# Kernel tuning notes

Measured on AMD Instinct MI355X. Metric: run time of the kernel, lower is better.

The kernel has to match this reference:

```python
import jax, jax.numpy as jnp
import numpy as np

B, H, S, D = 2, 16, 2048, 64

def setup_inputs() -> dict:
    key = jax.random.key(0)
    kq, kk, kv, km = jax.random.split(key, 4)
    q = jax.random.normal(kq, (B, H, S, D), dtype=jnp.float32)
    k = jax.random.normal(kk, (B, H, S, D), dtype=jnp.float32)
    v = jax.random.normal(kv, (B, H, S, D), dtype=jnp.float32)
    mask = jax.random.randint(km, (1, 1, S, S), 0, 2, dtype=jnp.int32)
    return {"q": q, "k": k, "v": v, "mask": mask}

def reference(q, k, v, mask):
    d_k = q.shape[-1]
    # scores: [B,H,S,S] = q @ k^T / sqrt(d_k)
    scores = jnp.einsum('bhqd,bhkd->bhqk', q, k) / jnp.sqrt(jnp.float32(d_k))
    scores = jnp.where(mask == 0, -jnp.inf, scores)
    score = jax.nn.softmax(scores, axis=-1)
    output = jnp.einsum('bhqk,bhkd->bhqd', score, v)
    return (output, score)
```

## Files before the change

kernel.cpp:

```cpp
#include <hip/hip_runtime.h>
#include <hip/hip_bf16.h>


#define BH 32
#define SEQ 2048
#define DIM 64

typedef __attribute__((ext_vector_type(8))) short short8;
typedef __attribute__((ext_vector_type(4))) float floatx4;
typedef __attribute__((ext_vector_type(4))) unsigned int uintx4;

__device__ __forceinline__ short f2bf(float f) {
    unsigned u = __builtin_bit_cast(unsigned, f);
    unsigned r = u + 0x7fffu + ((u >> 16) & 1u);
    return (short)(r >> 16);
}

__device__ __forceinline__ unsigned pack2bf(float lo, float hi) {
    unsigned ul = __builtin_bit_cast(unsigned, lo);
    unsigned uh = __builtin_bit_cast(unsigned, hi);
    ul = ul + 0x7fffu + ((ul >> 16) & 1u);
    uh = uh + 0x7fffu + ((uh >> 16) & 1u);
    return (ul >> 16) | (uh & 0xffff0000u);
}

__device__ __forceinline__ short8 cvt_frag(float4 a, float4 b) {
    short8 r;
    r[0] = f2bf(a.x); r[1] = f2bf(a.y); r[2] = f2bf(a.z); r[3] = f2bf(a.w);
    r[4] = f2bf(b.x); r[5] = f2bf(b.y); r[6] = f2bf(b.z); r[7] = f2bf(b.w);
    return r;
}

__device__ __forceinline__ short8 load_frag_f32(const float* p) {
    float4 a = *reinterpret_cast<const float4*>(p);
    float4 b = *reinterpret_cast<const float4*>(p + 4);
    return cvt_frag(a, b);
}


__global__ void maskbits_kernel(const int* __restrict__ mask,
                                unsigned long long* __restrict__ bits) {
    int tid = blockIdx.x * blockDim.x + threadIdx.x;
    unsigned long long b = __ballot(mask[tid] != 0);
    if ((threadIdx.x & 63) == 0) bits[tid >> 6] = b;
}

__global__ void cvt_k_kernel(const float* __restrict__ k, short* __restrict__ kb) {
    size_t i = ((size_t)blockIdx.x * blockDim.x + threadIdx.x) * 8;
    float4 a = *reinterpret_cast<const float4*>(k + i);
    float4 b = *reinterpret_cast<const float4*>(k + i + 4);
    *reinterpret_cast<short8*>(kb + i) = cvt_frag(a, b);
}

__global__ __launch_bounds__(256) void cvt_vt_kernel(const float* __restrict__ v,
                                                     short* __restrict__ vt) {
    __shared__ float tile[64][65];
    const int bh = blockIdx.y;
    const int sblk = blockIdx.x;
    const int t = threadIdx.x;
    const float* vb = v + ((size_t)bh * SEQ + sblk * 64) * DIM;
#pragma unroll
    for (int it = 0; it < 4; ++it) {
        int row = it * 16 + (t >> 4);
        int c4 = (t & 15) * 4;
        float4 a = *reinterpret_cast<const float4*>(vb + row * DIM + c4);
        tile[row][c4] = a.x; tile[row][c4 + 1] = a.y;
        tile[row][c4 + 2] = a.z; tile[row][c4 + 3] = a.w;
    }
    __syncthreads();
    short* vo = vt + (size_t)bh * SEQ * DIM;
#pragma unroll
    for (int it = 0; it < 2; ++it) {
        int c = it * 256 + t;
        int d = c >> 3;
        int s8 = (c & 7) * 8;
        short8 r;
#pragma unroll
        for (int j = 0; j < 8; ++j) r[j] = f2bf(tile[s8 + j][d]);
        *reinterpret_cast<short8*>(vo + (size_t)d * SEQ + sblk * 64 + s8) = r;
    }
}


__global__ __launch_bounds__(256, 8) void attn_fast(
    const float* __restrict__ q, const short* __restrict__ kb,
    const short* __restrict__ vt, const unsigned int* __restrict__ maskbits,
    float* __restrict__ out, float* __restrict__ score)
{
    __shared__ float lpart[4][16];
    __shared__ float ocomb[2][4][4][64];

    const int bh   = blockIdx.y;
    const int qb   = blockIdx.x;
    const int wave = threadIdx.x >> 6;
    const int lane = threadIdx.x & 63;
    const int quad = lane >> 4;
    const int n    = lane & 15;
    const int half = wave & 1;
    const int q0   = qb * 32 + (wave >> 1) * 16;
    const int q4   = quad * 4;
    const int cp0  = half * (SEQ / 64);
    const int cp1  = cp0 + (SEQ / 64);

    const float* qbase = q  + (size_t)bh * SEQ * DIM;
    const short* kbb   = kb + (size_t)bh * SEQ * DIM;
    const short* vtb   = vt + (size_t)bh * SEQ * DIM;

    const short8 qf0 = load_frag_f32(qbase + (size_t)(q0 + n) * DIM + quad * 8);
    const short8 qf1 = load_frag_f32(qbase + (size_t)(q0 + n) * DIM + 32 + quad * 8);

    const short* kn  = kbb + (size_t)n * DIM + quad * 8;
    const short* vn0 = vtb + (size_t)n * SEQ + quad * 8;
    const unsigned int* mr = maskbits + (size_t)(q0 + n) * (SEQ / 32);
    float* sb = score + (size_t)bh * SEQ * SEQ + (size_t)(q0 + n) * SEQ + q4;

    float lsum = 0.f;
    for (int cp = cp0; cp < cp1; ++cp) {
        const int cbase = cp * 32;
        const short* k0 = kn + (size_t)cbase * DIM;
        short8 kf00 = *reinterpret_cast<const short8*>(k0);
        short8 kf01 = *reinterpret_cast<const short8*>(k0 + 32);
        short8 kf10 = *reinterpret_cast<const short8*>(k0 + 16 * DIM);
        short8 kf11 = *reinterpret_cast<const short8*>(k0 + 16 * DIM + 32);
        floatx4 a0 = {0.f, 0.f, 0.f, 0.f}, a1 = {0.f, 0.f, 0.f, 0.f};
        a0 = __builtin_amdgcn_mfma_f32_16x16x32_bf16(kf00, qf0, a0, 0, 0, 0);
        a0 = __builtin_amdgcn_mfma_f32_16x16x32_bf16(kf01, qf1, a0, 0, 0, 0);
        a1 = __builtin_amdgcn_mfma_f32_16x16x32_bf16(kf10, qf0, a1, 0, 0, 0);
        a1 = __builtin_amdgcn_mfma_f32_16x16x32_bf16(kf11, qf1, a1, 0, 0, 0);
        const unsigned w = mr[cp];
#pragma unroll
        for (int r = 0; r < 4; ++r) {
            float e0 = ((w >> (q4 + r)) & 1u)      ? __expf(a0[r] * 0.125f) : 0.f;
            float e1 = ((w >> (q4 + r + 16)) & 1u) ? __expf(a1[r] * 0.125f) : 0.f;
            lsum += e0 + e1;
        }
    }
    lsum += __shfl_xor(lsum, 16, 64);
    lsum += __shfl_xor(lsum, 32, 64);
    if (lane < 16) lpart[wave][lane] = lsum;
    __syncthreads();
    const float invl = 1.0f / (lsum + lpart[wave ^ 1][n]);

    floatx4 o[4];
#pragma unroll
    for (int t = 0; t < 4; ++t) o[t] = (floatx4){0.f, 0.f, 0.f, 0.f};

    for (int cp = cp0; cp < cp1; ++cp) {
        const int cbase = cp * 32;
        const short* k0 = kn + (size_t)cbase * DIM;
        short8 kf00 = *reinterpret_cast<const short8*>(k0);
        short8 kf01 = *reinterpret_cast<const short8*>(k0 + 32);
        short8 kf10 = *reinterpret_cast<const short8*>(k0 + 16 * DIM);
        short8 kf11 = *reinterpret_cast<const short8*>(k0 + 16 * DIM + 32);
        floatx4 a0 = {0.f, 0.f, 0.f, 0.f}, a1 = {0.f, 0.f, 0.f, 0.f};
        a0 = __builtin_amdgcn_mfma_f32_16x16x32_bf16(kf00, qf0, a0, 0, 0, 0);
        a0 = __builtin_amdgcn_mfma_f32_16x16x32_bf16(kf01, qf1, a0, 0, 0, 0);
        a1 = __builtin_amdgcn_mfma_f32_16x16x32_bf16(kf10, qf0, a1, 0, 0, 0);
        a1 = __builtin_amdgcn_mfma_f32_16x16x32_bf16(kf11, qf1, a1, 0, 0, 0);
        const unsigned w = mr[cp];
        float p0[4], p1[4];
#pragma unroll
        for (int r = 0; r < 4; ++r) {
            float e0 = ((w >> (q4 + r)) & 1u)      ? __expf(a0[r] * 0.125f) : 0.f;
            float e1 = ((w >> (q4 + r + 16)) & 1u) ? __expf(a1[r] * 0.125f) : 0.f;
            p0[r] = e0 * invl;
            p1[r] = e1 * invl;
        }
        *reinterpret_cast<float4*>(sb + cbase)      = make_float4(p0[0], p0[1], p0[2], p0[3]);
        *reinterpret_cast<float4*>(sb + cbase + 16) = make_float4(p1[0], p1[1], p1[2], p1[3]);

        unsigned a0L = pack2bf(p0[0], p0[1]);
        unsigned a0H = pack2bf(p0[2], p0[3]);
        unsigned a1L = pack2bf(p1[0], p1[1]);
        unsigned a1H = pack2bf(p1[2], p1[3]);
        asm("v_permlane32_swap_b32 %0, %1" : "+v"(a0L), "+v"(a1L));
        asm("v_permlane16_swap_b32 %0, %1" : "+v"(a0L), "+v"(a1L));
        asm("v_permlane32_swap_b32 %0, %1" : "+v"(a0H), "+v"(a1H));
        asm("v_permlane16_swap_b32 %0, %1" : "+v"(a0H), "+v"(a1H));
        uintx4 pu = {a0L, a0H, a1L, a1H};
        short8 pf = __builtin_bit_cast(short8, pu);

#pragma unroll
        for (int t = 0; t < 4; ++t) {
            short8 vf = *reinterpret_cast<const short8*>(vn0 + (size_t)t * 16 * SEQ + cbase);
            o[t] = __builtin_amdgcn_mfma_f32_16x16x32_bf16(pf, vf, o[t], 0, 0, 0);
        }
    }

    if (half) {
#pragma unroll
        for (int t = 0; t < 4; ++t)
#pragma unroll
            for (int r = 0; r < 4; ++r)
                ocomb[wave >> 1][t][r][lane] = o[t][r];
    }
    __syncthreads();
    if (!half) {
        float* obase = out + ((size_t)bh * SEQ + q0) * DIM;
#pragma unroll
        for (int t = 0; t < 4; ++t)
#pragma unroll
            for (int r = 0; r < 4; ++r)
                obase[(size_t)(quad * 4 + r) * DIM + t * 16 + n] =
                    o[t][r] + ocomb[wave >> 1][t][r][lane];
    }
}


__global__ __launch_bounds__(256) void attn_ref(
    const float* __restrict__ q, const float* __restrict__ k,
    const float* __restrict__ v, const int* __restrict__ mask,
    const unsigned int* __restrict__ maskbits, int use_bits,
    float* __restrict__ out, float* __restrict__ score)
{
    __shared__ float plds[4][16][36];
    const int bh   = blockIdx.y;
    const int qb   = blockIdx.x;
    const int wave = threadIdx.x >> 6;
    const int lane = threadIdx.x & 63;
    const int quad = lane >> 4;
    const int n    = lane & 15;
    const int q0   = qb * 64 + wave * 16;
    const float* qbase = q + (size_t)bh * SEQ * DIM;
    const float* kbase = k + (size_t)bh * SEQ * DIM;
    const float* vbase = v + (size_t)bh * SEQ * DIM;
    const short8 qf0 = load_frag_f32(qbase + (size_t)(q0 + n) * DIM + quad * 8);
    const short8 qf1 = load_frag_f32(qbase + (size_t)(q0 + n) * DIM + 32 + quad * 8);
    float l[4] = {0.f, 0.f, 0.f, 0.f};
    for (int ct = 0; ct < SEQ / 16; ++ct) {
        const int col0 = ct * 16;
        short8 kf0 = load_frag_f32(kbase + (size_t)(col0 + n) * DIM + quad * 8);
        short8 kf1 = load_frag_f32(kbase + (size_t)(col0 + n) * DIM + 32 + quad * 8);
        floatx4 acc = {0.f, 0.f, 0.f, 0.f};
        acc = __builtin_amdgcn_mfma_f32_16x16x32_bf16(qf0, kf0, acc, 0, 0, 0);
        acc = __builtin_amdgcn_mfma_f32_16x16x32_bf16(qf1, kf1, acc, 0, 0, 0);
#pragma unroll
        for (int r = 0; r < 4; ++r) {
            const int row = q0 + quad * 4 + r;
            int mbit;
            if (use_bits) {
                unsigned w = maskbits[((size_t)row * SEQ + col0) >> 5];
                mbit = (w >> ((col0 & 31) + n)) & 1;
            } else {
                mbit = (mask[(size_t)row * SEQ + col0 + n] != 0);
            }
            l[r] += mbit ? __expf(acc[r] * 0.125f) : 0.0f;
        }
    }
#pragma unroll
    for (int r = 0; r < 4; ++r) {
        float x = l[r];
        x += __shfl_xor(x, 1, 64);
        x += __shfl_xor(x, 2, 64);
        x += __shfl_xor(x, 4, 64);
        x += __shfl_xor(x, 8, 64);
        l[r] = 1.0f / x;
    }
    floatx4 o[4];
#pragma unroll
    for (int t = 0; t < 4; ++t) o[t] = (floatx4){0.f, 0.f, 0.f, 0.f};
    float* srow = score + (size_t)bh * SEQ * SEQ;
    for (int cp = 0; cp < SEQ / 32; ++cp) {
        const int cbase = cp * 32;
#pragma unroll
        for (int half = 0; half < 2; ++half) {
            const int col0 = cbase + half * 16;
            short8 kf0 = load_frag_f32(kbase + (size_t)(col0 + n) * DIM + quad * 8);
            short8 kf1 = load_frag_f32(kbase + (size_t)(col0 + n) * DIM + 32 + quad * 8);
            floatx4 acc = {0.f, 0.f, 0.f, 0.f};
            acc = __builtin_amdgcn_mfma_f32_16x16x32_bf16(qf0, kf0, acc, 0, 0, 0);
            acc = __builtin_amdgcn_mfma_f32_16x16x32_bf16(qf1, kf1, acc, 0, 0, 0);
#pragma unroll
            for (int r = 0; r < 4; ++r) {
                const int row = q0 + quad * 4 + r;
                int mbit;
                if (use_bits) {
                    unsigned w = maskbits[((size_t)row * SEQ + col0) >> 5];
                    mbit = (w >> ((col0 & 31) + n)) & 1;
                } else {
                    mbit = (mask[(size_t)row * SEQ + col0 + n] != 0);
                }
                float e = mbit ? __expf(acc[r] * 0.125f) : 0.0f;
                float p = e * l[r];
                srow[(size_t)row * SEQ + col0 + n] = p;
                plds[wave][quad * 4 + r][half * 16 + n] = p;
            }
        }
        short8 pf = load_frag_f32(&plds[wave][n][quad * 8]);
#pragma unroll
        for (int t = 0; t < 4; ++t) {
            short8 vf;
#pragma unroll
            for (int j = 0; j < 8; ++j)
                vf[j] = f2bf(vbase[(size_t)(cbase + quad * 8 + j) * DIM + t * 16 + n]);
            o[t] = __builtin_amdgcn_mfma_f32_16x16x32_bf16(pf, vf, o[t], 0, 0, 0);
        }
    }
    float* obase = out + ((size_t)bh * SEQ + q0) * DIM;
#pragma unroll
    for (int t = 0; t < 4; ++t)
#pragma unroll
        for (int r = 0; r < 4; ++r)
            obase[(size_t)(quad * 4 + r) * DIM + t * 16 + n] = o[t][r];
}


extern "C" void kernel_launch(void* const* d_in, const int* in_sizes, int n_in,
                              void* d_out, int out_size, void* d_ws, size_t ws_size,
                              hipStream_t stream) {
    const float* q    = (const float*)d_in[0];
    const float* k    = (const float*)d_in[1];
    const float* v    = (const float*)d_in[2];
    const int*   mask = (const int*)d_in[3];

    float* out   = (float*)d_out;
    float* score = out + (size_t)BH * SEQ * DIM;

    const size_t bits_bytes = (size_t)SEQ * SEQ / 8;
    const size_t kb_bytes   = (size_t)BH * SEQ * DIM * 2;
    const size_t need_fast  = bits_bytes + 2 * kb_bytes;

    if (ws_size >= need_fast) {
        unsigned long long* bits = (unsigned long long*)d_ws;
        short* kbuf = (short*)((char*)d_ws + bits_bytes);
        short* vtb  = (short*)((char*)d_ws + bits_bytes + kb_bytes);

        maskbits_kernel<<<(SEQ * SEQ) / 256, 256, 0, stream>>>(mask, bits);
        cvt_k_kernel<<<(BH * SEQ * DIM / 8) / 256, 256, 0, stream>>>(k, kbuf);
        cvt_vt_kernel<<<dim3(SEQ / 64, BH), 256, 0, stream>>>(v, vtb);

        dim3 grid(SEQ / 32, BH);
        attn_fast<<<grid, 256, 0, stream>>>(q, kbuf, vtb,
                                            (const unsigned int*)d_ws, out, score);
    } else {
        const int use_bits = (ws_size >= bits_bytes) ? 1 : 0;
        if (use_bits)
            maskbits_kernel<<<(SEQ * SEQ) / 256, 256, 0, stream>>>(
                mask, (unsigned long long*)d_ws);
        dim3 grid(SEQ / 64, BH);
        attn_ref<<<grid, 256, 0, stream>>>(q, k, v, mask,
                                           (const unsigned int*)d_ws, use_bits,
                                           out, score);
    }
}
```

Before: 929.4 us.

## Stage score tiles in LDS for coalesced row stores, split keys across four waves

```diff
diff --git a/kernel.cpp b/kernel.cpp
--- a/kernel.cpp
+++ b/kernel.cpp
@@ -82,13 +82,13 @@
 }
 
 
-__global__ __launch_bounds__(256, 8) void attn_fast(
+__global__ __launch_bounds__(256, 4) void attn_fast(
     const float* __restrict__ q, const short* __restrict__ kb,
     const short* __restrict__ vt, const unsigned int* __restrict__ maskbits,
     float* __restrict__ out, float* __restrict__ score)
 {
+    __shared__ float ptile[16][516];
     __shared__ float lpart[4][16];
-    __shared__ float ocomb[2][4][4][64];
 
     const int bh   = blockIdx.y;
     const int qb   = blockIdx.x;
@@ -96,11 +96,8 @@
     const int lane = threadIdx.x & 63;
     const int quad = lane >> 4;
     const int n    = lane & 15;
-    const int half = wave & 1;
-    const int q0   = qb * 32 + (wave >> 1) * 16;
+    const int q0   = qb * 16;
     const int q4   = quad * 4;
-    const int cp0  = half * (SEQ / 64);
-    const int cp1  = cp0 + (SEQ / 64);
 
     const float* qbase = q  + (size_t)bh * SEQ * DIM;
     const short* kbb   = kb + (size_t)bh * SEQ * DIM;
@@ -112,10 +109,11 @@
     const short* kn  = kbb + (size_t)n * DIM + quad * 8;
     const short* vn0 = vtb + (size_t)n * SEQ + quad * 8;
     const unsigned int* mr = maskbits + (size_t)(q0 + n) * (SEQ / 32);
-    float* sb = score + (size_t)bh * SEQ * SEQ + (size_t)(q0 + n) * SEQ + q4;
+
 
     float lsum = 0.f;
-    for (int cp = cp0; cp < cp1; ++cp) {
+    for (int i = 0; i < 16; ++i) {
+        const int cp = ((i >> 2) * 16) + ((i & 3) * 4) + wave;
         const int cbase = cp * 32;
         const short* k0 = kn + (size_t)cbase * DIM;
         short8 kf00 = *reinterpret_cast<const short8*>(k0);
@@ -139,70 +137,94 @@
     lsum += __shfl_xor(lsum, 32, 64);
     if (lane < 16) lpart[wave][lane] = lsum;
     __syncthreads();
-    const float invl = 1.0f / (lsum + lpart[wave ^ 1][n]);
+    const float invl = 1.0f / (lpart[0][n] + lpart[1][n] + lpart[2][n] + lpart[3][n]);
 
     floatx4 o[4];
 #pragma unroll
     for (int t = 0; t < 4; ++t) o[t] = (floatx4){0.f, 0.f, 0.f, 0.f};
 
-    for (int cp = cp0; cp < cp1; ++cp) {
-        const int cbase = cp * 32;
-        const short* k0 = kn + (size_t)cbase * DIM;
-        short8 kf00 = *reinterpret_cast<const short8*>(k0);
-        short8 kf01 = *reinterpret_cast<const short8*>(k0 + 32);
-        short8 kf10 = *reinterpret_cast<const short8*>(k0 + 16 * DIM);
-        short8 kf11 = *reinterpret_cast<const short8*>(k0 + 16 * DIM + 32);
-        floatx4 a0 = {0.f, 0.f, 0.f, 0.f}, a1 = {0.f, 0.f, 0.f, 0.f};
-        a0 = __builtin_amdgcn_mfma_f32_16x16x32_bf16(kf00, qf0, a0, 0, 0, 0);
-        a0 = __builtin_amdgcn_mfma_f32_16x16x32_bf16(kf01, qf1, a0, 0, 0, 0);
-        a1 = __builtin_amdgcn_mfma_f32_16x16x32_bf16(kf10, qf0, a1, 0, 0, 0);
-        a1 = __builtin_amdgcn_mfma_f32_16x16x32_bf16(kf11, qf1, a1, 0, 0, 0);
-        const unsigned w = mr[cp];
-        float p0[4], p1[4];
-#pragma unroll
-        for (int r = 0; r < 4; ++r) {
-            float e0 = ((w >> (q4 + r)) & 1u)      ? __expf(a0[r] * 0.125f) : 0.f;
-            float e1 = ((w >> (q4 + r + 16)) & 1u) ? __expf(a1[r] * 0.125f) : 0.f;
-            p0[r] = e0 * invl;
-            p1[r] = e1 * invl;
-        }
-        *reinterpret_cast<float4*>(sb + cbase)      = make_float4(p0[0], p0[1], p0[2], p0[3]);
-        *reinterpret_cast<float4*>(sb + cbase + 16) = make_float4(p1[0], p1[1], p1[2], p1[3]);
-
-        unsigned a0L = pack2bf(p0[0], p0[1]);
-        unsigned a0H = pack2bf(p0[2], p0[3]);
-        unsigned a1L = pack2bf(p1[0], p1[1]);
-        unsigned a1H = pack2bf(p1[2], p1[3]);
-        asm("v_permlane32_swap_b32 %0, %1" : "+v"(a0L), "+v"(a1L));
-        asm("v_permlane16_swap_b32 %0, %1" : "+v"(a0L), "+v"(a1L));
-        asm("v_permlane32_swap_b32 %0, %1" : "+v"(a0H), "+v"(a1H));
-        asm("v_permlane16_swap_b32 %0, %1" : "+v"(a0H), "+v"(a1H));
-        uintx4 pu = {a0L, a0H, a1L, a1H};
-        short8 pf = __builtin_bit_cast(short8, pu);
-
-#pragma unroll
-        for (int t = 0; t < 4; ++t) {
-            short8 vf = *reinterpret_cast<const short8*>(vn0 + (size_t)t * 16 * SEQ + cbase);
-            o[t] = __builtin_amdgcn_mfma_f32_16x16x32_bf16(pf, vf, o[t], 0, 0, 0);
-        }
-    }
-
-    if (half) {
+    for (int g = 0; g < 4; ++g) {
+#pragma unroll
+        for (int j = 0; j < 4; ++j) {
+            const int cp = g * 16 + j * 4 + wave;
+            const int cbase = cp * 32;
+            const int lc = (j * 4 + wave) * 32;
+            const short* k0 = kn + (size_t)cbase * DIM;
+            short8 kf00 = *reinterpret_cast<const short8*>(k0);
+            short8 kf01 = *reinterpret_cast<const short8*>(k0 + 32);
+            short8 kf10 = *reinterpret_cast<const short8*>(k0 + 16 * DIM);
+            short8 kf11 = *reinterpret_cast<const short8*>(k0 + 16 * DIM + 32);
+            floatx4 a0 = {0.f, 0.f, 0.f, 0.f}, a1 = {0.f, 0.f, 0.f, 0.f};
+            a0 = __builtin_amdgcn_mfma_f32_16x16x32_bf16(kf00, qf0, a0, 0, 0, 0);
+            a0 = __builtin_amdgcn_mfma_f32_16x16x32_bf16(kf01, qf1, a0, 0, 0, 0);
+            a1 = __builtin_amdgcn_mfma_f32_16x16x32_bf16(kf10, qf0, a1, 0, 0, 0);
+            a1 = __builtin_amdgcn_mfma_f32_16x16x32_bf16(kf11, qf1, a1, 0, 0, 0);
+            const unsigned w = mr[cp];
+            float p0[4], p1[4];
+#pragma unroll
+            for (int r = 0; r < 4; ++r) {
+                float e0 = ((w >> (q4 + r)) & 1u)      ? __expf(a0[r] * 0.125f) : 0.f;
+                float e1 = ((w >> (q4 + r + 16)) & 1u) ? __expf(a1[r] * 0.125f) : 0.f;
+                p0[r] = e0 * invl;
+                p1[r] = e1 * invl;
+            }
+            *reinterpret_cast<float4*>(&ptile[n][lc + q4]) =
+                make_float4(p0[0], p0[1], p0[2], p0[3]);
+            *reinterpret_cast<float4*>(&ptile[n][lc + q4 + 16]) =
+                make_float4(p1[0], p1[1], p1[2], p1[3]);
+
+            unsigned a0L = pack2bf(p0[0], p0[1]);
+            unsigned a0H = pack2bf(p0[2], p0[3]);
+            unsigned a1L = pack2bf(p1[0], p1[1]);
+            unsigned a1H = pack2bf(p1[2], p1[3]);
+            asm("v_permlane32_swap_b32 %0, %1" : "+v"(a0L), "+v"(a1L));
+            asm("v_permlane16_swap_b32 %0, %1" : "+v"(a0L), "+v"(a1L));
+            asm("v_permlane32_swap_b32 %0, %1" : "+v"(a0H), "+v"(a1H));
+            asm("v_permlane16_swap_b32 %0, %1" : "+v"(a0H), "+v"(a1H));
+            uintx4 pu = {a0L, a0H, a1L, a1H};
+            short8 pf = __builtin_bit_cast(short8, pu);
+
+#pragma unroll
+            for (int t = 0; t < 4; ++t) {
+                short8 vf = *reinterpret_cast<const short8*>(
+                    vn0 + (size_t)t * 16 * SEQ + cbase);
+                o[t] = __builtin_amdgcn_mfma_f32_16x16x32_bf16(pf, vf, o[t], 0, 0, 0);
+            }
+        }
+        __syncthreads();
+        {
+            const int r = threadIdx.x >> 4;
+            const int c = (threadIdx.x & 15) * 4;
+            float* srow = score + (size_t)bh * SEQ * SEQ +
+                          (size_t)(q0 + r) * SEQ + g * 512;
+#pragma unroll
+            for (int i2 = 0; i2 < 8; ++i2)
+                *reinterpret_cast<float4*>(srow + c + i2 * 64) =
+                    *reinterpret_cast<const float4*>(&ptile[r][c + i2 * 64]);
+        }
+        __syncthreads();
+    }
+
+    float* ob = &ptile[0][0];
+    if (wave != 0) {
 #pragma unroll
         for (int t = 0; t < 4; ++t)
 #pragma unroll
             for (int r = 0; r < 4; ++r)
-                ocomb[wave >> 1][t][r][lane] = o[t][r];
+                ob[((wave - 1) * 16 + t * 4 + r) * 64 + lane] = o[t][r];
     }
     __syncthreads();
-    if (!half) {
+    if (wave == 0) {
         float* obase = out + ((size_t)bh * SEQ + q0) * DIM;
 #pragma unroll
         for (int t = 0; t < 4; ++t)
 #pragma unroll
-            for (int r = 0; r < 4; ++r)
-                obase[(size_t)(quad * 4 + r) * DIM + t * 16 + n] =
-                    o[t][r] + ocomb[wave >> 1][t][r][lane];
+            for (int r = 0; r < 4; ++r) {
+                const int s = t * 4 + r;
+                float vsum = o[t][r] + ob[s * 64 + lane] +
+                             ob[(16 + s) * 64 + lane] + ob[(32 + s) * 64 + lane];
+                obase[(size_t)(q4 + r) * DIM + t * 16 + n] = vsum;
+            }
     }
 }
 
@@ -329,7 +351,7 @@
         cvt_k_kernel<<<(BH * SEQ * DIM / 8) / 256, 256, 0, stream>>>(k, kbuf);
         cvt_vt_kernel<<<dim3(SEQ / 64, BH), 256, 0, stream>>>(v, vtb);
 
-        dim3 grid(SEQ / 32, BH);
+        dim3 grid(SEQ / 16, BH);
         attn_fast<<<grid, 256, 0, stream>>>(q, kbuf, vtb,
                                             (const unsigned int*)d_ws, out, score);
     } else {
```

Result: no change. 944.4 us (+1.6%).
